# Optimization experiments

Measured on AMD Instinct MI355X. Metric: run time of the kernel, lower is better.

## Reference

```python
import jax, jax.numpy as jnp
import numpy as np

S, X, G = 2048, 2048, 2
INPUT_SIZE = (3, 32, 32)
F = int(np.prod(INPUT_SIZE))


def setup_inputs() -> dict:
    key = jax.random.key(0)
    k1, k2, k3 = jax.random.split(key, 3)
    samples = jax.random.normal(k1, (S,) + INPUT_SIZE, dtype=jnp.float32)
    x = jax.random.normal(k2, (X,) + INPUT_SIZE, dtype=jnp.float32)
    # per-feature std per gradation, kept in [0.1, 1.0) like ranges_std scaling
    std = jax.random.uniform(k3, (G, F), dtype=jnp.float32, minval=0.1, maxval=1.0)
    return {"samples": samples, "x": x, "std": std}


def reference(samples, x, std):
    # samples: [S, C, H, W], x: [X, C, H, W], std: [G, F]
    G_, F_ = std.shape
    s = samples.reshape(samples.shape[0], F_)  # [S, F]
    xf = x.reshape(x.shape[0], F_)             # [X, F]
    w = 1.0 / (std * std)                       # [G, F] precision
    # per-gradation normalizer: -0.5*F*log(2pi) - sum_f log(std)
    const = -0.5 * F_ * jnp.log(2.0 * jnp.pi) - jnp.sum(jnp.log(std), axis=1)  # [G]
    # sum_f -0.5*((s-x)/std)^2 expanded: -0.5*(s^2 w - 2 s w x + x^2 w)
    A = jnp.einsum('sf,gf->gs', s * s, w)        # [G, S]
    C = jnp.einsum('xf,gf->gx', xf * xf, w)      # [G, X]
    B = jnp.einsum('sf,gf,xf->gsx', s, w, xf)    # [G, S, X] cross term
    logits = -0.5 * (A[:, :, None] - 2.0 * B + C[:, None, :]) + const[:, None, None]
    lp = jax.nn.logsumexp(logits, axis=2)        # over x (mixture components)
    lp = jax.nn.logsumexp(lp, axis=0)            # over gradations
    return lp - jnp.log(jnp.float32(x.shape[0] * G_))
```

## Files before the change

kernel.cpp:

```cpp
#include <hip/hip_runtime.h>
#include <math.h>
#include <stdint.h>

#define S_N 2048
#define X_N 2048
#define G_N 2
#define F_N 3072

#define TM 256
#define TN 128
#define BK 64
#define ITERS (F_N / BK)
#define NBUF 3

typedef __bf16 bf16;
typedef __bf16 bf16x4 __attribute__((ext_vector_type(4)));
typedef __bf16 bf16x8 __attribute__((ext_vector_type(8)));
typedef float f32x4 __attribute__((ext_vector_type(4)));
typedef int i32x4 __attribute__((ext_vector_type(4)));

__device__ __forceinline__ void gload_lds16(const bf16* g, void* l) {
  __builtin_amdgcn_global_load_lds(
      (const __attribute__((address_space(1))) void*)g,
      (__attribute__((address_space(3))) void*)l, 16, 0, 0);
}

__global__ __launch_bounds__(512) void k_prep(
    const float* __restrict__ samples, const float* __restrict__ xin,
    const float* __restrict__ stdv,
    bf16* __restrict__ U, bf16* __restrict__ V,
    float* __restrict__ A, float* __restrict__ C) {
  __shared__ float rlds[12288];
  __shared__ float redp[16];
  int t = threadIdx.x;
  int bid = blockIdx.x;
  int lane = t & 63, wv = t >> 6;

  for (int i = t; i < 2 * F_N; i += 512) {
    float v = stdv[i];
    rlds[6144 + i] = v;
    rlds[i] = 1.0f / v;
  }

  float sl0 = 0.f, sl1 = 0.f;
  for (int i = t; i < F_N; i += 512) {
    sl0 += logf(stdv[i]);
    sl1 += logf(stdv[F_N + i]);
  }
  for (int o = 32; o; o >>= 1) { sl0 += __shfl_xor(sl0, o); sl1 += __shfl_xor(sl1, o); }
  if (lane == 0) { redp[wv] = sl0; redp[8 + wv] = sl1; }
  __syncthreads();
  float t0 = 0.f, t1 = 0.f;
#pragma unroll
  for (int w2 = 0; w2 < 8; ++w2) { t0 += redp[w2]; t1 += redp[8 + w2]; }
  const float KLOG = -0.5f * (float)F_N * 1.8378770664093453f;
  float c0 = KLOG - t0, c1 = KLOG - t1;

  int l32 = t & 31;
  int rr = bid * 16 + (t >> 5);
  bool isS = rr < S_N;
  int rx = isS ? rr : rr - S_N;
  const float* src = isS ? samples + (size_t)rx * F_N : xin + (size_t)rx * F_N;

  if (isS) {
    bf16* d = U + (size_t)rx * F_N;
    float a0 = 0.f, a1 = 0.f;
#pragma unroll 4
    for (int k = 0; k < 24; ++k) {
      int c4 = l32 + k * 32;
      float4 sv = ((const float4*)src)[c4];
      float4 r0 = ((const float4*)rlds)[c4];
      float4 r1 = ((const float4*)rlds)[768 + c4];
      bf16x4 b;
      b[0] = (bf16)sv.x; b[1] = (bf16)sv.y; b[2] = (bf16)sv.z; b[3] = (bf16)sv.w;
      ((bf16x4*)d)[c4] = b;
      float f0 = (float)b[0], f1 = (float)b[1], f2 = (float)b[2], f3 = (float)b[3];
      a0 += f0 * f0 * (r0.x * r0.x) + f1 * f1 * (r0.y * r0.y)
          + f2 * f2 * (r0.z * r0.z) + f3 * f3 * (r0.w * r0.w);
      a1 += f0 * f0 * (r1.x * r1.x) + f1 * f1 * (r1.y * r1.y)
          + f2 * f2 * (r1.z * r1.z) + f3 * f3 * (r1.w * r1.w);
    }
    for (int o = 16; o; o >>= 1) { a0 += __shfl_xor(a0, o); a1 += __shfl_xor(a1, o); }
    if (l32 == 0) { A[rx] = a0 - 2.f * c0; A[S_N + rx] = a1 - 2.f * c1; }
  } else {
    bf16* d0 = V + (size_t)rx * F_N;
    bf16* d1 = V + ((size_t)X_N + rx) * F_N;
    const float* slds = rlds + 6144;
    float q0 = 0.f, q1 = 0.f;
#pragma unroll 4
    for (int k = 0; k < 24; ++k) {
      int c4 = l32 + k * 32;
      float4 xv = ((const float4*)src)[c4];
      float4 r0 = ((const float4*)rlds)[c4];
      float4 r1 = ((const float4*)rlds)[768 + c4];
      float4 s0 = ((const float4*)slds)[c4];
      float4 s1 = ((const float4*)slds)[768 + c4];
      bf16x4 y0, y1;
      y0[0] = (bf16)(xv.x * r0.x * r0.x); y0[1] = (bf16)(xv.y * r0.y * r0.y);
      y0[2] = (bf16)(xv.z * r0.z * r0.z); y0[3] = (bf16)(xv.w * r0.w * r0.w);
      y1[0] = (bf16)(xv.x * r1.x * r1.x); y1[1] = (bf16)(xv.y * r1.y * r1.y);
      y1[2] = (bf16)(xv.z * r1.z * r1.z); y1[3] = (bf16)(xv.w * r1.w * r1.w);
      ((bf16x4*)d0)[c4] = y0;
      ((bf16x4*)d1)[c4] = y1;
      float g0 = (float)y0[0] * s0.x, g1 = (float)y0[1] * s0.y;
      float g2 = (float)y0[2] * s0.z, g3 = (float)y0[3] * s0.w;
      q0 += g0 * g0 + g1 * g1 + g2 * g2 + g3 * g3;
      float h0 = (float)y1[0] * s1.x, h1 = (float)y1[1] * s1.y;
      float h2 = (float)y1[2] * s1.z, h3 = (float)y1[3] * s1.w;
      q1 += h0 * h0 + h1 * h1 + h2 * h2 + h3 * h3;
    }
    for (int o = 16; o; o >>= 1) { q0 += __shfl_xor(q0, o); q1 += __shfl_xor(q1, o); }
    if (l32 == 0) { C[rx] = q0; C[X_N + rx] = q1; }
  }
}

__global__ __launch_bounds__(512, 2) void k_gemm(const bf16* __restrict__ U, const bf16* __restrict__ V,
                                                 const float* __restrict__ A, const float* __restrict__ C,
                                                 float* __restrict__ logits) {
  __shared__ i32x4 lds[NBUF * 2048 + NBUF * 1024];
  i32x4* ldsA = lds;
  i32x4* ldsB = lds + NBUF * 2048;

  int t = threadIdx.x;
  int g = blockIdx.z;
  int bm = blockIdx.y * TM;
  int bn = blockIdx.x * TN;

  const bf16* Ub = U + (size_t)bm * F_N;
  const bf16* Vb = V + ((size_t)g * X_N + bn) * F_N;

  int wave = t >> 6, lane = t & 63;
  int pos = wave >> 1;
  int kh = wave & 1;
  int wm = pos >> 1;
  int wn = pos & 1;
  int r = lane & 15, q = lane >> 4;
  int fr = (r >> 1) & 7;
  int ck = (kh * 4 + q) ^ fr;
  int abase = (wm * 128 + r) * 8;
  int bbase = (wn * 64 + r) * 8;

  int row0 = t >> 3;
  int gcc = (t & 7) ^ ((t >> 4) & 7);
  const bf16* gA[4];
  const bf16* gB[2];
#pragma unroll
  for (int j = 0; j < 4; ++j) gA[j] = Ub + (size_t)(row0 + j * 64) * F_N + gcc * 8;
#pragma unroll
  for (int j = 0; j < 2; ++j) gB[j] = Vb + (size_t)(row0 + j * 64) * F_N + gcc * 8;

  f32x4 acc[8][4] = {};
  bf16x8 af[8], bfr[4];

#pragma unroll
  for (int j = 0; j < 4; ++j) gload_lds16(gA[j], &ldsA[0 * 2048 + t + j * 512]);
#pragma unroll
  for (int j = 0; j < 2; ++j) gload_lds16(gB[j], &ldsB[0 * 1024 + t + j * 512]);
#pragma unroll
  for (int j = 0; j < 4; ++j) gload_lds16(gA[j] + BK, &ldsA[1 * 2048 + t + j * 512]);
#pragma unroll
  for (int j = 0; j < 2; ++j) gload_lds16(gB[j] + BK, &ldsB[1 * 1024 + t + j * 512]);
  asm volatile("s_waitcnt vmcnt(6)" ::: "memory");
  __builtin_amdgcn_s_barrier();
  __builtin_amdgcn_sched_barrier(0);
#pragma unroll
  for (int ni = 0; ni < 4; ++ni)
    bfr[ni] = __builtin_bit_cast(bf16x8, ldsB[bbase + ni * 128 + ck]);
#pragma unroll
  for (int mi = 0; mi < 8; ++mi)
    af[mi] = __builtin_bit_cast(bf16x8, ldsA[abase + mi * 128 + ck]);

  int cur = 0;
  for (int it = 0; it < ITERS; ++it) {
    int k2 = it + 2;
    int pk = (k2 < ITERS ? k2 : 0) * BK;
    int stg = (cur >= 1) ? cur - 1 : 2;
    int nxt = (cur == 2) ? 0 : cur + 1;
    const i32x4* LAn = ldsA + nxt * 2048;
    const i32x4* LBn = ldsB + nxt * 1024;

    gload_lds16(gA[0] + pk, &ldsA[stg * 2048 + t]);
    gload_lds16(gA[1] + pk, &ldsA[stg * 2048 + t + 512]);
    gload_lds16(gA[2] + pk, &ldsA[stg * 2048 + t + 1024]);
    gload_lds16(gA[3] + pk, &ldsA[stg * 2048 + t + 1536]);
    gload_lds16(gB[0] + pk, &ldsB[stg * 1024 + t]);
    gload_lds16(gB[1] + pk, &ldsB[stg * 1024 + t + 512]);

    __builtin_amdgcn_s_setprio(1);
#pragma unroll
    for (int ni = 0; ni < 4; ++ni)
#pragma unroll
      for (int mi = 0; mi < 8; ++mi)
        acc[mi][ni] = __builtin_amdgcn_mfma_f32_16x16x32_bf16(af[mi], bfr[ni], acc[mi][ni], 0, 0, 0);
    __builtin_amdgcn_s_setprio(0);

    asm volatile("s_waitcnt vmcnt(6)" ::: "memory");
    __builtin_amdgcn_s_barrier();
    __builtin_amdgcn_sched_barrier(0);
#pragma unroll
    for (int ni = 0; ni < 4; ++ni)
      bfr[ni] = __builtin_bit_cast(bf16x8, LBn[bbase + ni * 128 + ck]);
#pragma unroll
    for (int mi = 0; mi < 8; ++mi)
      af[mi] = __builtin_bit_cast(bf16x8, LAn[abase + mi * 128 + ck]);

    cur = nxt;
  }

  asm volatile("s_waitcnt vmcnt(0) lgkmcnt(0)" ::: "memory");
  __builtin_amdgcn_s_barrier();

  f32x4* scr = (f32x4*)lds;
  {
    f32x4* mw = scr + wave * 1024;
    if (kh == 0) {
#pragma unroll
      for (int mi = 0; mi < 8; ++mi)
#pragma unroll
        for (int nl = 0; nl < 2; ++nl)
          mw[(mi * 2 + nl) * 64 + lane] = acc[mi][2 + nl];
    } else {
#pragma unroll
      for (int mi = 0; mi < 8; ++mi)
#pragma unroll
        for (int nl = 0; nl < 2; ++nl)
          mw[(mi * 2 + nl) * 64 + lane] = acc[mi][nl];
    }
  }
  __syncthreads();
  {
    const f32x4* pw = scr + (wave ^ 1) * 1024;
    if (kh == 0) {
#pragma unroll
      for (int mi = 0; mi < 8; ++mi)
#pragma unroll
        for (int nl = 0; nl < 2; ++nl)
          acc[mi][nl] += pw[(mi * 2 + nl) * 64 + lane];
    } else {
#pragma unroll
      for (int mi = 0; mi < 8; ++mi)
#pragma unroll
        for (int nl = 0; nl < 2; ++nl)
          acc[mi][2 + nl] += pw[(mi * 2 + nl) * 64 + lane];
    }
  }

  const float* Ap = A + (size_t)g * S_N + bm + wm * 128;
  const float* Cp = C + (size_t)g * X_N + bn + wn * 64 + kh * 32;
  float cv[2];
  cv[0] = Cp[r]; cv[1] = Cp[16 + r];
#pragma unroll
  for (int mi = 0; mi < 8; ++mi) {
#pragma unroll
    for (int i = 0; i < 4; ++i) {
      int rowl = mi * 16 + q * 4 + i;
      float av = Ap[rowl];
      float* orow = logits + ((size_t)g * S_N + bm + wm * 128 + rowl) * X_N + bn + wn * 64 + kh * 32;
      if (kh == 0) {
        orow[r]      = acc[mi][0][i] - 0.5f * (av + cv[0]);
        orow[16 + r] = acc[mi][1][i] - 0.5f * (av + cv[1]);
      } else {
        orow[r]      = acc[mi][2][i] - 0.5f * (av + cv[0]);
        orow[16 + r] = acc[mi][3][i] - 0.5f * (av + cv[1]);
      }
    }
  }
}

__global__ void k_lse(const float* __restrict__ logits, float* __restrict__ out) {
  int s = blockIdx.x, t = threadIdx.x;
  const float4* p0 = (const float4*)(logits + (size_t)s * X_N);
  const float4* p1 = (const float4*)(logits + ((size_t)S_N + s) * X_N);
  float4 v[4];
  v[0] = p0[t]; v[1] = p0[t + 256];
  v[2] = p1[t]; v[3] = p1[t + 256];

  float m = v[0].x;
#pragma unroll
  for (int j = 0; j < 4; ++j) {
    m = fmaxf(m, v[j].x); m = fmaxf(m, v[j].y);
    m = fmaxf(m, v[j].z); m = fmaxf(m, v[j].w);
  }
  for (int o = 32; o; o >>= 1) m = fmaxf(m, __shfl_xor(m, o));
  __shared__ float redm[4];
  __shared__ float reds[4];
  int w = t >> 6, l = t & 63;
  if (l == 0) redm[w] = m;
  __syncthreads();
  m = fmaxf(fmaxf(redm[0], redm[1]), fmaxf(redm[2], redm[3]));

  float sum = 0.f;
#pragma unroll
  for (int j = 0; j < 4; ++j) {
    sum += expf(v[j].x - m) + expf(v[j].y - m) + expf(v[j].z - m) + expf(v[j].w - m);
  }
  for (int o = 32; o; o >>= 1) sum += __shfl_xor(sum, o);
  if (l == 0) reds[w] = sum;
  __syncthreads();
  if (t == 0) {
    float tot = reds[0] + reds[1] + reds[2] + reds[3];
    out[s] = m + logf(tot) - 8.317766166719343f;
  }
}

extern "C" void kernel_launch(void* const* d_in, const int* in_sizes, int n_in,
                              void* d_out, int out_size, void* d_ws, size_t ws_size,
                              hipStream_t stream) {
  const float* samples = (const float*)d_in[0];
  const float* xin     = (const float*)d_in[1];
  const float* stdv    = (const float*)d_in[2];
  float* out = (float*)d_out;

  char* ws = (char*)d_ws;
  size_t off = 0;
  bf16* U = (bf16*)(ws + off);        off += (size_t)S_N * F_N * 2;
  bf16* V = (bf16*)(ws + off);        off += (size_t)G_N * X_N * F_N * 2;
  float* logits = (float*)(ws + off); off += (size_t)G_N * S_N * X_N * 4;
  float* A = (float*)(ws + off);      off += (size_t)G_N * S_N * 4;
  float* C = (float*)(ws + off);      off += (size_t)G_N * X_N * 4;

  k_prep<<<dim3(256), dim3(512), 0, stream>>>(samples, xin, stdv, U, V, A, C);
  k_gemm<<<dim3(X_N / TN, S_N / TM, G_N), dim3(512), 0, stream>>>(U, V, A, C, logits);
  k_lse<<<dim3(S_N), dim3(256), 0, stream>>>(logits, out);
}
```

Before: 152.2 us.

## Load GEMM A operand directly from global into double-buffered registers

Stops staging the A tile through LDS and instead has each wave load its A fragments straight from global memory into registers. The registers are ping-ponged between two buffers, with the loop unrolled by two, while B keeps its three-stage LDS pipeline. This removes LDS traffic and LDS space for A, but the two waves that share the same M rows now fetch A from global twice. It also raises VGPR pressure and leaves more global-load latency to be hidden by the MFMA work.

After: 217.6 us. 1.43x slower.

```diff
diff --git a/kernel.cpp b/kernel.cpp
--- a/kernel.cpp
+++ b/kernel.cpp
@@ -117,16 +117,14 @@
 __global__ __launch_bounds__(512, 2) void k_gemm(const bf16* __restrict__ U, const bf16* __restrict__ V,
                                                  const float* __restrict__ A, const float* __restrict__ C,
                                                  float* __restrict__ logits) {
-  __shared__ i32x4 lds[NBUF * 2048 + NBUF * 1024];
-  i32x4* ldsA = lds;
-  i32x4* ldsB = lds + NBUF * 2048;
+  __shared__ i32x4 lds[8192];
+  i32x4* ldsB = lds;
 
   int t = threadIdx.x;
   int g = blockIdx.z;
   int bm = blockIdx.y * TM;
   int bn = blockIdx.x * TN;
 
-  const bf16* Ub = U + (size_t)bm * F_N;
   const bf16* Vb = V + ((size_t)g * X_N + bn) * F_N;
 
   int wave = t >> 6, lane = t & 63;
@@ -137,75 +135,69 @@
   int r = lane & 15, q = lane >> 4;
   int fr = (r >> 1) & 7;
   int ck = (kh * 4 + q) ^ fr;
-  int abase = (wm * 128 + r) * 8;
   int bbase = (wn * 64 + r) * 8;
+
+  const bf16* gAr = U + (size_t)(bm + wm * 128 + r) * F_N + kh * 32 + q * 8;
 
   int row0 = t >> 3;
   int gcc = (t & 7) ^ ((t >> 4) & 7);
-  const bf16* gA[4];
   const bf16* gB[2];
 #pragma unroll
-  for (int j = 0; j < 4; ++j) gA[j] = Ub + (size_t)(row0 + j * 64) * F_N + gcc * 8;
-#pragma unroll
   for (int j = 0; j < 2; ++j) gB[j] = Vb + (size_t)(row0 + j * 64) * F_N + gcc * 8;
 
   f32x4 acc[8][4] = {};
-  bf16x8 af[8], bfr[4];
-
-#pragma unroll
-  for (int j = 0; j < 4; ++j) gload_lds16(gA[j], &ldsA[0 * 2048 + t + j * 512]);
-#pragma unroll
-  for (int j = 0; j < 2; ++j) gload_lds16(gB[j], &ldsB[0 * 1024 + t + j * 512]);
-#pragma unroll
-  for (int j = 0; j < 4; ++j) gload_lds16(gA[j] + BK, &ldsA[1 * 2048 + t + j * 512]);
-#pragma unroll
-  for (int j = 0; j < 2; ++j) gload_lds16(gB[j] + BK, &ldsB[1 * 1024 + t + j * 512]);
-  asm volatile("s_waitcnt vmcnt(6)" ::: "memory");
+  bf16x8 afA[8], afB[8], bfr[4];
+
+  gload_lds16(gB[0], &ldsB[0 * 1024 + t]);
+  gload_lds16(gB[1], &ldsB[0 * 1024 + t + 512]);
+  gload_lds16(gB[0] + BK, &ldsB[1 * 1024 + t]);
+  gload_lds16(gB[1] + BK, &ldsB[1 * 1024 + t + 512]);
+#pragma unroll
+  for (int mi = 0; mi < 8; ++mi)
+    afA[mi] = *(const bf16x8*)(gAr + (size_t)mi * 16 * F_N);
+  asm volatile("s_waitcnt vmcnt(14)" ::: "memory");
   __builtin_amdgcn_s_barrier();
   __builtin_amdgcn_sched_barrier(0);
 #pragma unroll
   for (int ni = 0; ni < 4; ++ni)
     bfr[ni] = __builtin_bit_cast(bf16x8, ldsB[bbase + ni * 128 + ck]);
-#pragma unroll
-  for (int mi = 0; mi < 8; ++mi)
-    af[mi] = __builtin_bit_cast(bf16x8, ldsA[abase + mi * 128 + ck]);
-
-  int cur = 0;
-  for (int it = 0; it < ITERS; ++it) {
-    int k2 = it + 2;
-    int pk = (k2 < ITERS ? k2 : 0) * BK;
-    int stg = (cur >= 1) ? cur - 1 : 2;
-    int nxt = (cur == 2) ? 0 : cur + 1;
-    const i32x4* LAn = ldsA + nxt * 2048;
-    const i32x4* LBn = ldsB + nxt * 1024;
-
-    gload_lds16(gA[0] + pk, &ldsA[stg * 2048 + t]);
-    gload_lds16(gA[1] + pk, &ldsA[stg * 2048 + t + 512]);
-    gload_lds16(gA[2] + pk, &ldsA[stg * 2048 + t + 1024]);
-    gload_lds16(gA[3] + pk, &ldsA[stg * 2048 + t + 1536]);
-    gload_lds16(gB[0] + pk, &ldsB[stg * 1024 + t]);
-    gload_lds16(gB[1] + pk, &ldsB[stg * 1024 + t + 512]);
-
-    __builtin_amdgcn_s_setprio(1);
-#pragma unroll
-    for (int ni = 0; ni < 4; ++ni)
-#pragma unroll
-      for (int mi = 0; mi < 8; ++mi)
-        acc[mi][ni] = __builtin_amdgcn_mfma_f32_16x16x32_bf16(af[mi], bfr[ni], acc[mi][ni], 0, 0, 0);
-    __builtin_amdgcn_s_setprio(0);
-
-    asm volatile("s_waitcnt vmcnt(6)" ::: "memory");
-    __builtin_amdgcn_s_barrier();
-    __builtin_amdgcn_sched_barrier(0);
-#pragma unroll
-    for (int ni = 0; ni < 4; ++ni)
-      bfr[ni] = __builtin_bit_cast(bf16x8, LBn[bbase + ni * 128 + ck]);
-#pragma unroll
-    for (int mi = 0; mi < 8; ++mi)
-      af[mi] = __builtin_bit_cast(bf16x8, LAn[abase + mi * 128 + ck]);
-
-    cur = nxt;
-  }
+
+#define ATILE(IT, A_CUR, A_NXT)                                                  \
+  {                                                                              \
+    int k2 = (IT) + 2;                                                           \
+    int pkB = (k2 < ITERS ? k2 : 0) * BK;    \
+    int k1 = (IT) + 1;                                                           \
+    int pkA = (k1 < ITERS ? k1 : 0) * BK;                                        \
+    int stg = ((IT) + 2) % 3;                                                    \
+    int nxt = ((IT) + 1) % 3;                                                    \
+                \
+    gload_lds16(gB[0] + pkB, &ldsB[stg * 1024 + t]);                             \
+    gload_lds16(gB[1] + pkB, &ldsB[stg * 1024 + t + 512]);                       \
+    _Pragma("unroll")                                                            \
+    for (int mi = 0; mi < 8; ++mi)                                               \
+      A_NXT[mi] = *(const bf16x8*)(gAr + (size_t)mi * 16 * F_N + pkA);           \
+           \
+    __builtin_amdgcn_s_setprio(1);                                               \
+    _Pragma("unroll")                                                            \
+    for (int ni = 0; ni < 4; ++ni)                                               \
+      _Pragma("unroll")                                                          \
+      for (int mi = 0; mi < 8; ++mi)                                             \
+        acc[mi][ni] = __builtin_amdgcn_mfma_f32_16x16x32_bf16(A_CUR[mi], bfr[ni], acc[mi][ni], 0, 0, 0); \
+    __builtin_amdgcn_s_setprio(0);                                               \
+        \
+    asm volatile("s_waitcnt vmcnt(14)" ::: "memory");                            \
+    __builtin_amdgcn_s_barrier();                                                \
+    __builtin_amdgcn_sched_barrier(0);                                           \
+    _Pragma("unroll")                                                            \
+    for (int ni = 0; ni < 4; ++ni)                                               \
+      bfr[ni] = __builtin_bit_cast(bf16x8, ldsB[nxt * 1024 + bbase + ni * 128 + ck]); \
+  }
+
+  for (int it0 = 0; it0 < ITERS; it0 += 2) {
+    ATILE(it0,     afA, afB)
+    ATILE(it0 + 1, afB, afA)
+  }
+#undef ATILE
 
   asm volatile("s_waitcnt vmcnt(0) lgkmcnt(0)" ::: "memory");
   __builtin_amdgcn_s_barrier();
```

## Shrink GEMM tile to 128x128 with BK 32 and drop intra-block split-K

Applied to the files above, without the earlier changes.

Reworks the bf16 GEMM kernel to use a 128x128 output tile, a 32-wide K step and 256 threads (4 waves, each computing a 64x64 sub-tile). The previous split-K across wave pairs is removed along with its LDS reduction in the epilogue. The LDS swizzle and load mapping are adjusted to match. This doubles the block count and cuts LDS per block, which should help occupancy, but each block reuses less data and runs twice as many K iterations, so there are more barriers per FLOP.

After: 163.4 us. 1.07x slower.

```diff
diff --git a/kernel.cpp b/kernel.cpp
--- a/kernel.cpp
+++ b/kernel.cpp
@@ -7,9 +7,9 @@
 #define G_N 2
 #define F_N 3072
 
-#define TM 256
+#define TM 128
 #define TN 128
-#define BK 64
+#define BK 32
 #define ITERS (F_N / BK)
 #define NBUF 3
 
@@ -114,12 +114,11 @@
   }
 }
 
-__global__ __launch_bounds__(512, 2) void k_gemm(const bf16* __restrict__ U, const bf16* __restrict__ V,
+__global__ __launch_bounds__(256, 2) void k_gemm(const bf16* __restrict__ U, const bf16* __restrict__ V,
                                                  const float* __restrict__ A, const float* __restrict__ C,
                                                  float* __restrict__ logits) {
-  __shared__ i32x4 lds[NBUF * 2048 + NBUF * 1024];
-  i32x4* ldsA = lds;
-  i32x4* ldsB = lds + NBUF * 2048;
+  __shared__ i32x4 ldsA[NBUF * 512];
+  __shared__ i32x4 ldsB[NBUF * 512];
 
   int t = threadIdx.x;
   int g = blockIdx.z;
@@ -130,45 +129,45 @@
   const bf16* Vb = V + ((size_t)g * X_N + bn) * F_N;
 
   int wave = t >> 6, lane = t & 63;
-  int pos = wave >> 1;
-  int kh = wave & 1;
-  int wm = pos >> 1;
-  int wn = pos & 1;
+  int wm = wave & 1, wn = wave >> 1;
   int r = lane & 15, q = lane >> 4;
-  int fr = (r >> 1) & 7;
-  int ck = (kh * 4 + q) ^ fr;
-  int abase = (wm * 128 + r) * 8;
-  int bbase = (wn * 64 + r) * 8;
-
-  int row0 = t >> 3;
-  int gcc = (t & 7) ^ ((t >> 4) & 7);
-  const bf16* gA[4];
+  int cs = (r >> 1) & 3;
+  int ck = q ^ cs;
+  int abase = (wm * 64 + r) * 4 + ck;
+  int bbase = (wn * 64 + r) * 4 + ck;
+
+  int row0 = t >> 2;
+  int gcc = (t & 3) ^ ((t >> 3) & 3);
+  const bf16* gA[2];
   const bf16* gB[2];
 #pragma unroll
-  for (int j = 0; j < 4; ++j) gA[j] = Ub + (size_t)(row0 + j * 64) * F_N + gcc * 8;
-#pragma unroll
-  for (int j = 0; j < 2; ++j) gB[j] = Vb + (size_t)(row0 + j * 64) * F_N + gcc * 8;
-
-  f32x4 acc[8][4] = {};
-  bf16x8 af[8], bfr[4];
-
-#pragma unroll
-  for (int j = 0; j < 4; ++j) gload_lds16(gA[j], &ldsA[0 * 2048 + t + j * 512]);
-#pragma unroll
-  for (int j = 0; j < 2; ++j) gload_lds16(gB[j], &ldsB[0 * 1024 + t + j * 512]);
-#pragma unroll
-  for (int j = 0; j < 4; ++j) gload_lds16(gA[j] + BK, &ldsA[1 * 2048 + t + j * 512]);
-#pragma unroll
-  for (int j = 0; j < 2; ++j) gload_lds16(gB[j] + BK, &ldsB[1 * 1024 + t + j * 512]);
-  asm volatile("s_waitcnt vmcnt(6)" ::: "memory");
+  for (int j = 0; j < 2; ++j) {
+    gA[j] = Ub + (size_t)(row0 + j * 64) * F_N + gcc * 8;
+    gB[j] = Vb + (size_t)(row0 + j * 64) * F_N + gcc * 8;
+  }
+
+  f32x4 acc[4][4] = {};
+  bf16x8 af[4], bfr[4];
+
+#pragma unroll
+  for (int j = 0; j < 2; ++j) {
+    gload_lds16(gA[j], &ldsA[0 * 512 + t + j * 256]);
+    gload_lds16(gB[j], &ldsB[0 * 512 + t + j * 256]);
+  }
+#pragma unroll
+  for (int j = 0; j < 2; ++j) {
+    gload_lds16(gA[j] + BK, &ldsA[1 * 512 + t + j * 256]);
+    gload_lds16(gB[j] + BK, &ldsB[1 * 512 + t + j * 256]);
+  }
+  asm volatile("s_waitcnt vmcnt(4)" ::: "memory");
   __builtin_amdgcn_s_barrier();
   __builtin_amdgcn_sched_barrier(0);
 #pragma unroll
   for (int ni = 0; ni < 4; ++ni)
-    bfr[ni] = __builtin_bit_cast(bf16x8, ldsB[bbase + ni * 128 + ck]);
-#pragma unroll
-  for (int mi = 0; mi < 8; ++mi)
-    af[mi] = __builtin_bit_cast(bf16x8, ldsA[abase + mi * 128 + ck]);
+    bfr[ni] = __builtin_bit_cast(bf16x8, ldsB[bbase + ni * 64]);
+#pragma unroll
+  for (int mi = 0; mi < 4; ++mi)
+    af[mi] = __builtin_bit_cast(bf16x8, ldsA[abase + mi * 64]);
 
   int cur = 0;
   for (int it = 0; it < ITERS; ++it) {
@@ -176,93 +175,52 @@
     int pk = (k2 < ITERS ? k2 : 0) * BK;
     int stg = (cur >= 1) ? cur - 1 : 2;
     int nxt = (cur == 2) ? 0 : cur + 1;
-    const i32x4* LAn = ldsA + nxt * 2048;
-    const i32x4* LBn = ldsB + nxt * 1024;
-
-    gload_lds16(gA[0] + pk, &ldsA[stg * 2048 + t]);
-    gload_lds16(gA[1] + pk, &ldsA[stg * 2048 + t + 512]);
-    gload_lds16(gA[2] + pk, &ldsA[stg * 2048 + t + 1024]);
-    gload_lds16(gA[3] + pk, &ldsA[stg * 2048 + t + 1536]);
-    gload_lds16(gB[0] + pk, &ldsB[stg * 1024 + t]);
-    gload_lds16(gB[1] + pk, &ldsB[stg * 1024 + t + 512]);
+    const i32x4* LAn = ldsA + nxt * 512;
+    const i32x4* LBn = ldsB + nxt * 512;
+
+    gload_lds16(gA[0] + pk, &ldsA[stg * 512 + t]);
+    gload_lds16(gA[1] + pk, &ldsA[stg * 512 + t + 256]);
+    gload_lds16(gB[0] + pk, &ldsB[stg * 512 + t]);
+    gload_lds16(gB[1] + pk, &ldsB[stg * 512 + t + 256]);
 
     __builtin_amdgcn_s_setprio(1);
 #pragma unroll
     for (int ni = 0; ni < 4; ++ni)
 #pragma unroll
-      for (int mi = 0; mi < 8; ++mi)
+      for (int mi = 0; mi < 4; ++mi)
         acc[mi][ni] = __builtin_amdgcn_mfma_f32_16x16x32_bf16(af[mi], bfr[ni], acc[mi][ni], 0, 0, 0);
     __builtin_amdgcn_s_setprio(0);
 
-    asm volatile("s_waitcnt vmcnt(6)" ::: "memory");
+    asm volatile("s_waitcnt vmcnt(4)" ::: "memory");
     __builtin_amdgcn_s_barrier();
     __builtin_amdgcn_sched_barrier(0);
 #pragma unroll
     for (int ni = 0; ni < 4; ++ni)
-      bfr[ni] = __builtin_bit_cast(bf16x8, LBn[bbase + ni * 128 + ck]);
-#pragma unroll
-    for (int mi = 0; mi < 8; ++mi)
-      af[mi] = __builtin_bit_cast(bf16x8, LAn[abase + mi * 128 + ck]);
+      bfr[ni] = __builtin_bit_cast(bf16x8, LBn[bbase + ni * 64]);
+#pragma unroll
+    for (int mi = 0; mi < 4; ++mi)
+      af[mi] = __builtin_bit_cast(bf16x8, LAn[abase + mi * 64]);
 
     cur = nxt;
   }
 
   asm volatile("s_waitcnt vmcnt(0) lgkmcnt(0)" ::: "memory");
-  __builtin_amdgcn_s_barrier();
-
-  f32x4* scr = (f32x4*)lds;
-  {
-    f32x4* mw = scr + wave * 1024;
-    if (kh == 0) {
-#pragma unroll
-      for (int mi = 0; mi < 8; ++mi)
-#pragma unroll
-        for (int nl = 0; nl < 2; ++nl)
-          mw[(mi * 2 + nl) * 64 + lane] = acc[mi][2 + nl];
-    } else {
-#pragma unroll
-      for (int mi = 0; mi < 8; ++mi)
-#pragma unroll
-        for (int nl = 0; nl < 2; ++nl)
-          mw[(mi * 2 + nl) * 64 + lane] = acc[mi][nl];
-    }
-  }
-  __syncthreads();
-  {
-    const f32x4* pw = scr + (wave ^ 1) * 1024;
-    if (kh == 0) {
-#pragma unroll
-      for (int mi = 0; mi < 8; ++mi)
-#pragma unroll
-        for (int nl = 0; nl < 2; ++nl)
-          acc[mi][nl] += pw[(mi * 2 + nl) * 64 + lane];
-    } else {
-#pragma unroll
-      for (int mi = 0; mi < 8; ++mi)
-#pragma unroll
-        for (int nl = 0; nl < 2; ++nl)
-          acc[mi][2 + nl] += pw[(mi * 2 + nl) * 64 + lane];
-    }
-  }
-
-  const float* Ap = A + (size_t)g * S_N + bm + wm * 128;
-  const float* Cp = C + (size_t)g * X_N + bn + wn * 64 + kh * 32;
-  float cv[2];
-  cv[0] = Cp[r]; cv[1] = Cp[16 + r];
-#pragma unroll
-  for (int mi = 0; mi < 8; ++mi) {
+
+  const float* Ap = A + (size_t)g * S_N + bm + wm * 64;
+  const float* Cp = C + (size_t)g * X_N + bn + wn * 64;
+  float cv[4];
+#pragma unroll
+  for (int ni = 0; ni < 4; ++ni) cv[ni] = Cp[ni * 16 + r];
+#pragma unroll
+  for (int mi = 0; mi < 4; ++mi) {
 #pragma unroll
     for (int i = 0; i < 4; ++i) {
       int rowl = mi * 16 + q * 4 + i;
       float av = Ap[rowl];
-      float* orow = logits + ((size_t)g * S_N + bm + wm * 128 + rowl) * X_N + bn + wn * 64 + kh * 32;
-      if (kh == 0) {
-        orow[r]      = acc[mi][0][i] - 0.5f * (av + cv[0]);
-        orow[16 + r] = acc[mi][1][i] - 0.5f * (av + cv[1]);
-      } else {
-        orow[r]      = acc[mi][2][i] - 0.5f * (av + cv[0]);
-        orow[16 + r] = acc[mi][3][i] - 0.5f * (av + cv[1]);
-      }
+      float* orow = logits + ((size_t)g * S_N + bm + wm * 64 + rowl) * X_N + bn + wn * 64;
+#pragma unroll
+      for (int ni = 0; ni < 4; ++ni)
+        orow[ni * 16 + r] = acc[mi][ni][i] - 0.5f * (av + cv[ni]);
     }
   }
 }
@@ -320,6 +278,6 @@
   float* C = (float*)(ws + off);      off += (size_t)G_N * X_N * 4;
 
   k_prep<<<dim3(256), dim3(512), 0, stream>>>(samples, xin, stdv, U, V, A, C);
-  k_gemm<<<dim3(X_N / TN, S_N / TM, G_N), dim3(512), 0, stream>>>(U, V, A, C, logits);
+  k_gemm<<<dim3(X_N / TN, S_N / TM, G_N), dim3(256), 0, stream>>>(U, V, A, C, logits);
   k_lse<<<dim3(S_N), dim3(256), 0, stream>>>(logits, out);
 }
```
